# Performance work log

Hardware: AMD Instinct MI355X
Metric: run time of the kernel (lower is better)

Reference implementation:

```python
import jax, jax.numpy as jnp
import numpy as np

WIN = (7, 7)
NUM_HEADS = 12
DIM = 384
HEAD_DIM = DIM // NUM_HEADS
SCALE = HEAD_DIM ** (-0.5)


def _relative_position_index(wh, ww):
    coords = np.stack(np.meshgrid(np.arange(wh), np.arange(ww), indexing='ij'))  # (2, wh, ww)
    cf = coords.reshape(2, -1)                                                    # (2, N)
    rel = cf[:, :, None] - cf[:, None, :]                                         # (2, N, N)
    rel = rel.transpose(1, 2, 0).astype(np.int64)
    rel[:, :, 0] += wh - 1
    rel[:, :, 1] += ww - 1
    rel[:, :, 0] *= 2 * ww - 1
    return rel.sum(-1).astype(np.int32)                                           # (N, N)


def setup_inputs() -> dict:
    key = jax.random.key(0)
    ks = jax.random.split(key, 5)
    B_, N, C = 4096, WIN[0] * WIN[1], DIM
    nW = 1024
    x = jax.random.normal(ks[0], (B_, N, C), dtype=jnp.float32)
    mask = jnp.zeros((nW, N, N), dtype=jnp.float32)  # 0/-inf additive mask; zeros here
    qkv_w = jax.random.normal(ks[1], (C, 3 * C), dtype=jnp.float32) * 0.02
    qkv_b = jnp.zeros((3 * C,), dtype=jnp.float32)
    proj_w = jax.random.normal(ks[2], (C, C), dtype=jnp.float32) * 0.02
    proj_b = jnp.zeros((C,), dtype=jnp.float32)
    table_size = (2 * WIN[0] - 1) * (2 * WIN[1] - 1)
    rpb_table = jax.random.normal(ks[3], (table_size, NUM_HEADS), dtype=jnp.float32) * 0.02
    rel_index = jnp.asarray(_relative_position_index(*WIN))
    return {"x": x, "mask": mask, "qkv_w": qkv_w, "qkv_b": qkv_b,
            "proj_w": proj_w, "proj_b": proj_b, "rpb_table": rpb_table,
            "rel_index": rel_index}


def reference(x, mask, qkv_w, qkv_b, proj_w, proj_b, rpb_table, rel_index):
    B_, N, C = x.shape
    H, Dh = NUM_HEADS, HEAD_DIM
    qkv = x @ qkv_w + qkv_b                                   # (B_, N, 3C)
    qkv = qkv.reshape(B_, N, 3, H, Dh).transpose(2, 0, 3, 1, 4)
    q, k, v = qkv[0], qkv[1], qkv[2]                          # each (B_, H, N, Dh)
    attn = jnp.einsum('bhnd,bhmd->bhnm', q * SCALE, k)        # (B_, H, N, N)
    # gathered relative position bias -> (H, N, N)
    bias = rpb_table[rel_index.reshape(-1)].reshape(N, N, H).transpose(2, 0, 1)
    attn = attn + bias[None]
    nW = mask.shape[0]
    attn = attn.reshape(B_ // nW, nW, H, N, N) + mask[None, :, None]
    attn = attn.reshape(B_, H, N, N)
    attn = jax.nn.softmax(attn, axis=-1)
    out = jnp.einsum('bhnm,bhmd->bhnd', attn, v)              # (B_, H, N, Dh)
    out = out.transpose(0, 2, 1, 3).reshape(B_, N, C)
    return out @ proj_w + proj_b
```

## Files before the change

kernel.cpp:

```cpp
#include <hip/hip_runtime.h>


#define NWIN 4096
#define NW_MASK 1024
#define NH 12
#define DIM 384
#define HD 32
#define NT 49
#define SCALEF 0.17677669529663687f

typedef __attribute__((ext_vector_type(4))) float f32x4;
typedef __attribute__((ext_vector_type(8))) __bf16 bf16x8;
typedef __attribute__((ext_vector_type(4))) unsigned int u32x4;

#define MFMA16(A, B, C) __builtin_amdgcn_mfma_f32_16x16x32_bf16( \
    __builtin_bit_cast(bf16x8, A), __builtin_bit_cast(bf16x8, B), (C), 0, 0, 0)

__device__ __forceinline__ void split2(float x0, float x1, unsigned& h, unsigned& l) {
    unsigned b0 = __float_as_uint(x0), b1 = __float_as_uint(x1);
    unsigned m0 = b0 & 0xffff0000u, m1 = b1 & 0xffff0000u;
    h = m1 | (m0 >> 16);
    float r0 = x0 - __uint_as_float(m0);
    float r1 = x1 - __uint_as_float(m1);
    l = (__float_as_uint(r1) & 0xffff0000u) | (__float_as_uint(r0) >> 16);
}

__device__ __forceinline__ void cvt8(const float4& a, const float4& c,
                                     u32x4& hi, u32x4& lo) {
    unsigned h0, l0, h1, l1, h2, l2, h3, l3;
    split2(a.x, a.y, h0, l0);
    split2(a.z, a.w, h1, l1);
    split2(c.x, c.y, h2, l2);
    split2(c.z, c.w, h3, l3);
    hi = u32x4{h0, h1, h2, h3};
    lo = u32x4{l0, l1, l2, l3};
}

__global__ __launch_bounds__(256)
void conv_w(const float* __restrict__ qkv_w, const float* __restrict__ proj_w,
            u32x4* __restrict__ wf)
{
    int tg = blockIdx.x * 256 + threadIdx.x;
    int fid = tg >> 6, lane = tg & 63;
    int kt = fid / 96, ntc = fid - kt * 96;
    const float* src; int ncols, n; u32x4* dst;
    if (ntc < 72) {
        src = qkv_w; ncols = 3 * DIM; n = ntc * 16 + (lane & 15);
        dst = wf + (size_t)((kt * 72 + ntc) * 128);
    } else {
        int nt2 = ntc - 72;
        src = proj_w; ncols = DIM; n = nt2 * 16 + (lane & 15);
        dst = wf + (size_t)(12 * 72 * 128) + (size_t)((kt * 24 + nt2) * 128);
    }
    int k0 = kt * 32 + ((lane >> 4) << 3);
    float e[8];
    #pragma unroll
    for (int j = 0; j < 8; ++j) e[j] = src[(size_t)(k0 + j) * ncols + n];
    float4 a = make_float4(e[0], e[1], e[2], e[3]);
    float4 c = make_float4(e[4], e[5], e[6], e[7]);
    u32x4 hi, lo; cvt8(a, c, hi, lo);
    dst[lane] = hi; dst[64 + lane] = lo;
}

__global__ __launch_bounds__(256, 3)
void attn_mfma(const float* __restrict__ x,
               const float* __restrict__ mask,
               const float* __restrict__ qkv_b,
               const float* __restrict__ rpb,
               const int* __restrict__ rel,
               const u32x4* __restrict__ wf,
               float* __restrict__ y)
{
    __shared__ __align__(16) float qs[2][NT * 36];
    __shared__ __align__(16) float ks[2][NT * 36];
    __shared__ __align__(16) float vT[2][HD * 52];
    __shared__ __align__(16) float lg[NT * 52];

    const int b = blockIdx.x;
    const int t = threadIdx.x;
    const int lane = t & 63;
    const int wid = t >> 6;
    const int h_l = wid >> 1;
    const int mhalf = wid & 1;
    const int lrow = lane & 15;
    const int lk8 = (lane >> 4) << 3;
    const int lr4 = (lane >> 4) << 2;
    const float* xb = x + (size_t)b * (NT * DIM);
    const float* mrow = mask + (size_t)(b & (NW_MASK - 1)) * (NT * NT);
    const u32x4* wfl = wf + lane;

    for (int pass = 0; pass < 6; ++pass) {
        const int h = pass * 2 + h_l;
        int gnt[6];
        #pragma unroll
        for (int ln = 0; ln < 6; ++ln)
            gnt[ln] = (ln >> 1) * 24 + 2 * h + (ln & 1);

        f32x4 acc[2][6];
        #pragma unroll
        for (int mt = 0; mt < 2; ++mt)
            #pragma unroll
            for (int ln = 0; ln < 6; ++ln)
                acc[mt][ln] = f32x4{0.f, 0.f, 0.f, 0.f};

        for (int kt = 0; kt < 12; ++kt) {
            u32x4 ah[2], al[2];
            #pragma unroll
            for (int mt = 0; mt < 2; ++mt) {
                int row = mhalf * 32 + mt * 16 + lrow;
                float4 a = make_float4(0.f, 0.f, 0.f, 0.f);
                float4 c = make_float4(0.f, 0.f, 0.f, 0.f);
                if (row < NT) {
                    const float4* px = (const float4*)(xb + row * DIM + kt * 32 + lk8);
                    a = px[0]; c = px[1];
                }
                cvt8(a, c, ah[mt], al[mt]);
            }
            #pragma unroll
            for (int ln = 0; ln < 6; ++ln) {
                const u32x4* bp = wfl + (kt * 72 + gnt[ln]) * 128;
                u32x4 bh = bp[0], bl = bp[64];
                #pragma unroll
                for (int mt = 0; mt < 2; ++mt) {
                    acc[mt][ln] = MFMA16(al[mt], bh, acc[mt][ln]);
                    acc[mt][ln] = MFMA16(ah[mt], bl, acc[mt][ln]);
                    acc[mt][ln] = MFMA16(ah[mt], bh, acc[mt][ln]);
                }
            }
        }

        #pragma unroll
        for (int ln = 0; ln < 6; ++ln) {
            int cc = ln * 16 + lrow;
            int p = cc >> 5, d = cc & 31;
            float bias = qkv_b[p * DIM + h * HD + d];
            #pragma unroll
            for (int mt = 0; mt < 2; ++mt) {
                #pragma unroll
                for (int r = 0; r < 4; ++r) {
                    int row = mhalf * 32 + mt * 16 + lr4 + r;
                    if (row < NT) {
                        float v = acc[mt][ln][r] + bias;
                        if (p == 0)      qs[h_l][row * 36 + d] = v * SCALEF;
                        else if (p == 1) ks[h_l][row * 36 + d] = v;
                        else             vT[h_l][d * 52 + row] = v;
                    }
                }
            }
        }
        __syncthreads();

        for (int hh = 0; hh < 2; ++hh) {
            const int hg = pass * 2 + hh;
            for (int idx = t; idx < NT * NT; idx += 256) {
                int n = idx / NT, m = idx - n * NT;
                const float4* q4 = (const float4*)&qs[hh][n * 36];
                const float4* k4 = (const float4*)&ks[hh][m * 36];
                float s = 0.f;
                #pragma unroll
                for (int u = 0; u < 8; ++u) {
                    float4 qa = q4[u], ka = k4[u];
                    s += qa.x * ka.x + qa.y * ka.y + qa.z * ka.z + qa.w * ka.w;
                }
                s += rpb[rel[idx] * NH + hg] + mrow[idx];
                lg[n * 52 + m] = s;
            }
            __syncthreads();
            if (t < NT) {
                float mx = -1e30f;
                for (int m = 0; m < NT; ++m) mx = fmaxf(mx, lg[t * 52 + m]);
                float sum = 0.f;
                for (int m = 0; m < NT; ++m) {
                    float e = __expf(lg[t * 52 + m] - mx);
                    lg[t * 52 + m] = e; sum += e;
                }
                float inv = 1.f / sum;
                for (int m = 0; m < NT; ++m) lg[t * 52 + m] *= inv;
            }
            __syncthreads();
            for (int idx = t; idx < NT * HD; idx += 256) {
                int n = idx >> 5, dd = idx & 31;
                const float4* p4 = (const float4*)&lg[n * 52];
                const float4* v4 = (const float4*)&vT[hh][dd * 52];
                float s = 0.f;
                #pragma unroll
                for (int u = 0; u < 12; ++u) {
                    float4 pa = p4[u], va = v4[u];
                    s += pa.x * va.x + pa.y * va.y + pa.z * va.z + pa.w * va.w;
                }
                s += lg[n * 52 + 48] * vT[hh][dd * 52 + 48];
                y[((size_t)b * NT + n) * DIM + hg * HD + dd] = s;
            }
            __syncthreads();
        }
    }
}

__global__ __launch_bounds__(256)
void proj_mfma(const u32x4* __restrict__ pwf,
               const float* __restrict__ proj_b,
               float* __restrict__ y)
{
    const int t = threadIdx.x;
    const int lane = t & 63;
    const int wid = t >> 6;
    const int mhalf = wid >> 1, nhalf = wid & 1;
    const int lrow = lane & 15;
    const int lk8 = (lane >> 4) << 3;
    const int lr4 = (lane >> 4) << 2;
    float* yb = y + (size_t)blockIdx.x * (64 * DIM);
    const u32x4* pwl = pwf + lane;

    f32x4 acc[2][12];
    #pragma unroll
    for (int mt = 0; mt < 2; ++mt)
        #pragma unroll
        for (int ln = 0; ln < 12; ++ln)
            acc[mt][ln] = f32x4{0.f, 0.f, 0.f, 0.f};

    for (int kt = 0; kt < 12; ++kt) {
        u32x4 ah[2], al[2];
        #pragma unroll
        for (int mt = 0; mt < 2; ++mt) {
            int row = mhalf * 32 + mt * 16 + lrow;
            const float4* px = (const float4*)(yb + row * DIM + kt * 32 + lk8);
            float4 a = px[0], c = px[1];
            cvt8(a, c, ah[mt], al[mt]);
        }
        #pragma unroll
        for (int ln = 0; ln < 12; ++ln) {
            const u32x4* bp = pwl + (kt * 24 + nhalf * 12 + ln) * 128;
            u32x4 bh = bp[0], bl = bp[64];
            #pragma unroll
            for (int mt = 0; mt < 2; ++mt) {
                acc[mt][ln] = MFMA16(al[mt], bh, acc[mt][ln]);
                acc[mt][ln] = MFMA16(ah[mt], bl, acc[mt][ln]);
                acc[mt][ln] = MFMA16(ah[mt], bh, acc[mt][ln]);
            }
        }
    }
    __syncthreads();
    #pragma unroll
    for (int ln = 0; ln < 12; ++ln) {
        int col = (nhalf * 12 + ln) * 16 + lrow;
        float bias = proj_b[col];
        #pragma unroll
        for (int mt = 0; mt < 2; ++mt)
            #pragma unroll
            for (int r = 0; r < 4; ++r) {
                int row = mhalf * 32 + mt * 16 + lr4 + r;
                yb[row * DIM + col] = acc[mt][ln][r] + bias;
            }
    }
}

#define HD_P 33
#define CHUNK 128
#define THREADS_A 384

__global__ __launch_bounds__(THREADS_A)
void win_attn_kernel(const float* __restrict__ x,
                     const float* __restrict__ mask,
                     const float* __restrict__ qkv_w,
                     const float* __restrict__ qkv_b,
                     const float* __restrict__ rpb,
                     const int*   __restrict__ rel,
                     float* __restrict__ y)
{
    __shared__ float xs[NT * CHUNK];
    __shared__ float qs[NT * HD_P];
    __shared__ float ks_[NT * HD_P];
    __shared__ float vs[NT * HD_P];
    __shared__ float lg[NT * NT];

    const int b = blockIdx.x;
    const int t = threadIdx.x;
    const float* xb = x + (size_t)b * (NT * DIM);
    const float* mrow = mask + (size_t)(b & (NW_MASK - 1)) * (NT * NT);

    const int tx = t % 96;
    const int ty = t / 96;
    const int p  = tx / 32;
    const int d  = tx % 32;

    for (int h = 0; h < NH; ++h) {
        float acc[13];
        #pragma unroll
        for (int i = 0; i < 13; ++i) acc[i] = 0.f;
        const int wcol = p * DIM + h * HD + d;

        for (int c = 0; c < 3; ++c) {
            __syncthreads();
            for (int i = t; i < NT * (CHUNK / 4); i += THREADS_A) {
                int r = i >> 5;
                int j = i & 31;
                ((float4*)xs)[i] = ((const float4*)xb)[r * 96 + c * 32 + j];
            }
            __syncthreads();
            const float4* xs4 = (const float4*)xs;
            const float* wb = qkv_w + (size_t)(c * CHUNK) * (3 * DIM) + wcol;
            for (int kk4 = 0; kk4 < CHUNK / 4; ++kk4) {
                float w0 = wb[(size_t)(kk4 * 4 + 0) * (3 * DIM)];
                float w1 = wb[(size_t)(kk4 * 4 + 1) * (3 * DIM)];
                float w2 = wb[(size_t)(kk4 * 4 + 2) * (3 * DIM)];
                float w3 = wb[(size_t)(kk4 * 4 + 3) * (3 * DIM)];
                #pragma unroll
                for (int i = 0; i < 13; ++i) {
                    int r = ty + 4 * i;
                    if (r < NT) {
                        float4 xv = xs4[r * 32 + kk4];
                        acc[i] += xv.x * w0;
                        acc[i] += xv.y * w1;
                        acc[i] += xv.z * w2;
                        acc[i] += xv.w * w3;
                    }
                }
            }
        }
        float bv = qkv_b[wcol];
        float* dst = (p == 0) ? qs : (p == 1) ? ks_ : vs;
        #pragma unroll
        for (int i = 0; i < 13; ++i) {
            int r = ty + 4 * i;
            if (r < NT) dst[r * HD_P + d] = acc[i] + bv;
        }
        __syncthreads();

        for (int idx = t; idx < NT * NT; idx += THREADS_A) {
            int n = idx / NT, m = idx % NT;
            float s = 0.f;
            #pragma unroll
            for (int kk = 0; kk < HD; ++kk)
                s += qs[n * HD_P + kk] * ks_[m * HD_P + kk];
            s = s * SCALEF + rpb[rel[idx] * NH + h] + mrow[idx];
            lg[idx] = s;
        }
        __syncthreads();

        if (t < NT) {
            float mx = -1e30f;
            for (int m = 0; m < NT; ++m) mx = fmaxf(mx, lg[t * NT + m]);
            float sum = 0.f;
            for (int m = 0; m < NT; ++m) {
                float e = __expf(lg[t * NT + m] - mx);
                lg[t * NT + m] = e;
                sum += e;
            }
            float inv = 1.f / sum;
            for (int m = 0; m < NT; ++m) lg[t * NT + m] *= inv;
        }
        __syncthreads();

        for (int idx = t; idx < NT * HD; idx += THREADS_A) {
            int n = idx >> 5, dd = idx & 31;
            float s = 0.f;
            #pragma unroll
            for (int m = 0; m < NT; ++m)
                s += lg[n * NT + m] * vs[m * HD_P + dd];
            y[(size_t)b * (NT * DIM) + n * DIM + h * HD + dd] = s;
        }
    }
}

#define RPB 16
__global__ __launch_bounds__(384)
void proj_kernel(const float* __restrict__ proj_w,
                 const float* __restrict__ proj_b,
                 float* __restrict__ y)
{
    __shared__ float ys[RPB * DIM];
    const int t = threadIdx.x;
    float* base = y + (size_t)blockIdx.x * (RPB * DIM);
    for (int i = t; i < RPB * DIM / 4; i += 384)
        ((float4*)ys)[i] = ((const float4*)base)[i];
    __syncthreads();

    float acc[RPB];
    #pragma unroll
    for (int i = 0; i < RPB; ++i) acc[i] = 0.f;
    const float* wp = proj_w + t;
    const float4* ys4 = (const float4*)ys;
    for (int kk4 = 0; kk4 < DIM / 4; ++kk4) {
        float w0 = wp[(kk4 * 4 + 0) * DIM];
        float w1 = wp[(kk4 * 4 + 1) * DIM];
        float w2 = wp[(kk4 * 4 + 2) * DIM];
        float w3 = wp[(kk4 * 4 + 3) * DIM];
        #pragma unroll
        for (int i = 0; i < RPB; ++i) {
            float4 xv = ys4[i * 96 + kk4];
            acc[i] += xv.x * w0 + xv.y * w1 + xv.z * w2 + xv.w * w3;
        }
    }
    float bv = proj_b[t];
    #pragma unroll
    for (int i = 0; i < RPB; ++i)
        base[i * DIM + t] = acc[i] + bv;
}

extern "C" void kernel_launch(void* const* d_in, const int* in_sizes, int n_in,
                              void* d_out, int out_size, void* d_ws, size_t ws_size,
                              hipStream_t stream) {
    const float* x      = (const float*)d_in[0];
    const float* mask   = (const float*)d_in[1];
    const float* qkv_w  = (const float*)d_in[2];
    const float* qkv_b  = (const float*)d_in[3];
    const float* proj_w = (const float*)d_in[4];
    const float* proj_b = (const float*)d_in[5];
    const float* rpb    = (const float*)d_in[6];
    const int*   rel    = (const int*)d_in[7];
    float* out = (float*)d_out;

    const size_t WS_NEED = (size_t)(12 * 96 * 128) * 16;
    if (d_ws != nullptr && ws_size >= WS_NEED) {
        u32x4* wf = (u32x4*)d_ws;
        conv_w<<<288, 256, 0, stream>>>(qkv_w, proj_w, wf);
        attn_mfma<<<NWIN, 256, 0, stream>>>(x, mask, qkv_b, rpb, rel, wf, out);
        proj_mfma<<<(NWIN * NT) / 64, 256, 0, stream>>>(wf + (size_t)(12 * 72 * 128), proj_b, out);
    } else {
        win_attn_kernel<<<NWIN, THREADS_A, 0, stream>>>(x, mask, qkv_w, qkv_b, rpb, rel, out);
        proj_kernel<<<(NWIN * NT) / RPB, 384, 0, stream>>>(proj_w, proj_b, out);
    }
}
```

Before: 2.209 ms.

## Register-resident fused attention per head pair with fp16 QK dot products

Replaces the three shared-memory-synchronized phases (logits, single-thread-per-row softmax, PV) with one phase in which 8-thread groups own 4 query rows each. Both heads of a pass are processed at once, using fp16 Q/K with fdot2, shuffle-based softmax reductions and shuffle-broadcast PV accumulation. The relative position bias is pregathered into a per-head table inside the weight conversion kernel, which removes the indirect gather. This cuts barriers and serial softmax work, at the cost of fp16 precision on QK, more registers and some idle threads, since only 208 of 256 are active.

```diff
diff --git a/kernel.cpp b/kernel.cpp
--- a/kernel.cpp
+++ b/kernel.cpp
@@ -12,9 +12,26 @@
 typedef __attribute__((ext_vector_type(4))) float f32x4;
 typedef __attribute__((ext_vector_type(8))) __bf16 bf16x8;
 typedef __attribute__((ext_vector_type(4))) unsigned int u32x4;
+typedef __attribute__((ext_vector_type(2))) _Float16 h2;
 
 #define MFMA16(A, B, C) __builtin_amdgcn_mfma_f32_16x16x32_bf16( \
     __builtin_bit_cast(bf16x8, A), __builtin_bit_cast(bf16x8, B), (C), 0, 0, 0)
+
+#if defined(__has_builtin)
+#if __has_builtin(__builtin_amdgcn_fdot2)
+#define HAS_FDOT2 1
+#endif
+#endif
+
+__device__ __forceinline__ float fdot2u(unsigned a, unsigned b, float c) {
+#ifdef HAS_FDOT2
+    return __builtin_amdgcn_fdot2(__builtin_bit_cast(h2, a),
+                                  __builtin_bit_cast(h2, b), c, false);
+#else
+    h2 av = __builtin_bit_cast(h2, a), bv = __builtin_bit_cast(h2, b);
+    return c + (float)av.x * (float)bv.x + (float)av.y * (float)bv.y;
+#endif
+}
 
 __device__ __forceinline__ void split2(float x0, float x1, unsigned& h, unsigned& l) {
     unsigned b0 = __float_as_uint(x0), b1 = __float_as_uint(x1);
@@ -27,54 +44,62 @@
 
 __device__ __forceinline__ void cvt8(const float4& a, const float4& c,
                                      u32x4& hi, u32x4& lo) {
-    unsigned h0, l0, h1, l1, h2, l2, h3, l3;
+    unsigned h0, l0, h1, l1, h2_, l2, h3, l3;
     split2(a.x, a.y, h0, l0);
     split2(a.z, a.w, h1, l1);
-    split2(c.x, c.y, h2, l2);
+    split2(c.x, c.y, h2_, l2);
     split2(c.z, c.w, h3, l3);
-    hi = u32x4{h0, h1, h2, h3};
+    hi = u32x4{h0, h1, h2_, h3};
     lo = u32x4{l0, l1, l2, l3};
 }
 
 __global__ __launch_bounds__(256)
 void conv_w(const float* __restrict__ qkv_w, const float* __restrict__ proj_w,
-            u32x4* __restrict__ wf)
+            const float* __restrict__ rpb, const int* __restrict__ rel,
+            u32x4* __restrict__ wf, float* __restrict__ biasT)
 {
-    int tg = blockIdx.x * 256 + threadIdx.x;
-    int fid = tg >> 6, lane = tg & 63;
-    int kt = fid / 96, ntc = fid - kt * 96;
-    const float* src; int ncols, n; u32x4* dst;
-    if (ntc < 72) {
-        src = qkv_w; ncols = 3 * DIM; n = ntc * 16 + (lane & 15);
-        dst = wf + (size_t)((kt * 72 + ntc) * 128);
+    if (blockIdx.x < 288) {
+        int tg = blockIdx.x * 256 + threadIdx.x;
+        int fid = tg >> 6, lane = tg & 63;
+        int kt = fid / 96, ntc = fid - kt * 96;
+        const float* src; int ncols, n; u32x4* dst;
+        if (ntc < 72) {
+            src = qkv_w; ncols = 3 * DIM; n = ntc * 16 + (lane & 15);
+            dst = wf + (size_t)((kt * 72 + ntc) * 128);
+        } else {
+            int nt2 = ntc - 72;
+            src = proj_w; ncols = DIM; n = nt2 * 16 + (lane & 15);
+            dst = wf + (size_t)(12 * 72 * 128) + (size_t)((kt * 24 + nt2) * 128);
+        }
+        int k0 = kt * 32 + ((lane >> 4) << 3);
+        float e[8];
+        #pragma unroll
+        for (int j = 0; j < 8; ++j) e[j] = src[(size_t)(k0 + j) * ncols + n];
+        float4 a = make_float4(e[0], e[1], e[2], e[3]);
+        float4 c = make_float4(e[4], e[5], e[6], e[7]);
+        u32x4 hi, lo; cvt8(a, c, hi, lo);
+        dst[lane] = hi; dst[64 + lane] = lo;
     } else {
-        int nt2 = ntc - 72;
-        src = proj_w; ncols = DIM; n = nt2 * 16 + (lane & 15);
-        dst = wf + (size_t)(12 * 72 * 128) + (size_t)((kt * 24 + nt2) * 128);
-    }
-    int k0 = kt * 32 + ((lane >> 4) << 3);
-    float e[8];
-    #pragma unroll
-    for (int j = 0; j < 8; ++j) e[j] = src[(size_t)(k0 + j) * ncols + n];
-    float4 a = make_float4(e[0], e[1], e[2], e[3]);
-    float4 c = make_float4(e[4], e[5], e[6], e[7]);
-    u32x4 hi, lo; cvt8(a, c, hi, lo);
-    dst[lane] = hi; dst[64 + lane] = lo;
+        int tid = (blockIdx.x - 288) * 256 + threadIdx.x;
+        if (tid < NH * NT * NT) {
+            int h = tid / (NT * NT);
+            int idx = tid - h * (NT * NT);
+            biasT[tid] = rpb[rel[idx] * NH + h];
+        }
+    }
 }
 
 __global__ __launch_bounds__(256, 3)
 void attn_mfma(const float* __restrict__ x,
                const float* __restrict__ mask,
                const float* __restrict__ qkv_b,
-               const float* __restrict__ rpb,
-               const int* __restrict__ rel,
+               const float* __restrict__ biasT,
                const u32x4* __restrict__ wf,
                float* __restrict__ y)
 {
-    __shared__ __align__(16) float qs[2][NT * 36];
-    __shared__ __align__(16) float ks[2][NT * 36];
-    __shared__ __align__(16) float vT[2][HD * 52];
-    __shared__ __align__(16) float lg[NT * 52];
+    __shared__ __align__(16) _Float16 qs16[2][NT * 56];
+    __shared__ __align__(16) _Float16 ks16[2][NT * 56];
+    __shared__ __align__(16) float    vs[2][NT * 36];
 
     const int b = blockIdx.x;
     const int t = threadIdx.x;
@@ -89,6 +114,14 @@
     const float* mrow = mask + (size_t)(b & (NW_MASK - 1)) * (NT * NT);
     const u32x4* wfl = wf + lane;
 
+    const int g  = t >> 3;
+    const int j8 = t & 7;
+    const int hh = (g < 13) ? 0 : 1;
+    const int rq = g - hh * 13;
+    const int n0 = rq * 4;
+    const int nrows = (rq == 12) ? 1 : 4;
+    const bool act = g < 26;
+
     for (int pass = 0; pass < 6; ++pass) {
         const int h = pass * 2 + h_l;
         int gnt[6];
@@ -129,6 +162,8 @@
             }
         }
 
+        __syncthreads();
+
         #pragma unroll
         for (int ln = 0; ln < 6; ++ln) {
             int cc = ln * 16 + lrow;
@@ -141,62 +176,122 @@
                     int row = mhalf * 32 + mt * 16 + lr4 + r;
                     if (row < NT) {
                         float v = acc[mt][ln][r] + bias;
-                        if (p == 0)      qs[h_l][row * 36 + d] = v * SCALEF;
-                        else if (p == 1) ks[h_l][row * 36 + d] = v;
-                        else             vT[h_l][d * 52 + row] = v;
+                        if (p == 0)      qs16[h_l][row * 56 + d] = (_Float16)(v * SCALEF);
+                        else if (p == 1) ks16[h_l][row * 56 + d] = (_Float16)v;
+                        else             vs[h_l][row * 36 + d] = v;
                     }
                 }
             }
         }
         __syncthreads();
 
-        for (int hh = 0; hh < 2; ++hh) {
+        if (act) {
             const int hg = pass * 2 + hh;
-            for (int idx = t; idx < NT * NT; idx += 256) {
-                int n = idx / NT, m = idx - n * NT;
-                const float4* q4 = (const float4*)&qs[hh][n * 36];
-                const float4* k4 = (const float4*)&ks[hh][m * 36];
-                float s = 0.f;
+            const float* bT = biasT + hg * (NT * NT);
+
+            unsigned qreg[4][16];
+            #pragma unroll
+            for (int r = 0; r < 4; ++r) {
+                if (r < nrows) {
+                    const u32x4* qp = (const u32x4*)&qs16[hh][(n0 + r) * 56];
+                    #pragma unroll
+                    for (int w = 0; w < 4; ++w) {
+                        u32x4 qv = qp[w];
+                        qreg[r][w * 4 + 0] = qv[0];
+                        qreg[r][w * 4 + 1] = qv[1];
+                        qreg[r][w * 4 + 2] = qv[2];
+                        qreg[r][w * 4 + 3] = qv[3];
+                    }
+                }
+            }
+
+            float P[4][7];
+            #pragma unroll
+            for (int i = 0; i < 7; ++i) {
+                int m = j8 + 8 * i;
+                bool vm = m < NT;
+                u32x4 kw0{}, kw1{}, kw2{}, kw3{};
+                if (vm) {
+                    const u32x4* kp = (const u32x4*)&ks16[hh][m * 56];
+                    kw0 = kp[0]; kw1 = kp[1]; kw2 = kp[2]; kw3 = kp[3];
+                }
                 #pragma unroll
-                for (int u = 0; u < 8; ++u) {
-                    float4 qa = q4[u], ka = k4[u];
-                    s += qa.x * ka.x + qa.y * ka.y + qa.z * ka.z + qa.w * ka.w;
-                }
-                s += rpb[rel[idx] * NH + hg] + mrow[idx];
-                lg[n * 52 + m] = s;
-            }
-            __syncthreads();
-            if (t < NT) {
-                float mx = -1e30f;
-                for (int m = 0; m < NT; ++m) mx = fmaxf(mx, lg[t * 52 + m]);
-                float sum = 0.f;
-                for (int m = 0; m < NT; ++m) {
-                    float e = __expf(lg[t * 52 + m] - mx);
-                    lg[t * 52 + m] = e; sum += e;
-                }
-                float inv = 1.f / sum;
-                for (int m = 0; m < NT; ++m) lg[t * 52 + m] *= inv;
-            }
-            __syncthreads();
-            for (int idx = t; idx < NT * HD; idx += 256) {
-                int n = idx >> 5, dd = idx & 31;
-                const float4* p4 = (const float4*)&lg[n * 52];
-                const float4* v4 = (const float4*)&vT[hh][dd * 52];
-                float s = 0.f;
+                for (int r = 0; r < 4; ++r) {
+                    if (r < nrows) {
+                        float lv = -1e30f;
+                        if (vm) {
+                            float dsum = 0.f;
+                            #pragma unroll
+                            for (int c = 0; c < 4; ++c) dsum = fdot2u(qreg[r][c], kw0[c], dsum);
+                            #pragma unroll
+                            for (int c = 0; c < 4; ++c) dsum = fdot2u(qreg[r][4 + c], kw1[c], dsum);
+                            #pragma unroll
+                            for (int c = 0; c < 4; ++c) dsum = fdot2u(qreg[r][8 + c], kw2[c], dsum);
+                            #pragma unroll
+                            for (int c = 0; c < 4; ++c) dsum = fdot2u(qreg[r][12 + c], kw3[c], dsum);
+                            int idx = (n0 + r) * NT + m;
+                            lv = dsum + bT[idx] + mrow[idx];
+                        }
+                        P[r][i] = lv;
+                    }
+                }
+            }
+
+            #pragma unroll
+            for (int r = 0; r < 4; ++r) {
+                if (r < nrows) {
+                    float mx = P[r][0];
+                    #pragma unroll
+                    for (int i = 1; i < 7; ++i) mx = fmaxf(mx, P[r][i]);
+                    mx = fmaxf(mx, __shfl_xor(mx, 1, 8));
+                    mx = fmaxf(mx, __shfl_xor(mx, 2, 8));
+                    mx = fmaxf(mx, __shfl_xor(mx, 4, 8));
+                    float sm = 0.f;
+                    #pragma unroll
+                    for (int i = 0; i < 7; ++i) {
+                        float e = __expf(P[r][i] - mx);
+                        P[r][i] = e; sm += e;
+                    }
+                    sm += __shfl_xor(sm, 1, 8);
+                    sm += __shfl_xor(sm, 2, 8);
+                    sm += __shfl_xor(sm, 4, 8);
+                    float inv = 1.f / sm;
+                    #pragma unroll
+                    for (int i = 0; i < 7; ++i) P[r][i] *= inv;
+                }
+            }
+
+            f32x4 oacc[4];
+            #pragma unroll
+            for (int r = 0; r < 4; ++r) oacc[r] = f32x4{0.f, 0.f, 0.f, 0.f};
+            #pragma unroll
+            for (int i8 = 0; i8 < 7; ++i8) {
                 #pragma unroll
-                for (int u = 0; u < 12; ++u) {
-                    float4 pa = p4[u], va = v4[u];
-                    s += pa.x * va.x + pa.y * va.y + pa.z * va.z + pa.w * va.w;
-                }
-                s += lg[n * 52 + 48] * vT[hh][dd * 52 + 48];
-                y[((size_t)b * NT + n) * DIM + hg * HD + dd] = s;
-            }
-            __syncthreads();
-        }
-    }
-}
-
-__global__ __launch_bounds__(256)
+                for (int jj = 0; jj < 8; ++jj) {
+                    const int mm = i8 * 8 + jj;
+                    if (mm < NT) {
+                        f32x4 v4 = *(const f32x4*)&vs[hh][mm * 36 + j8 * 4];
+                        #pragma unroll
+                        for (int r = 0; r < 4; ++r) {
+                            if (r < nrows) {
+                                float p = __shfl(P[r][i8], jj, 8);
+                                oacc[r] += v4 * p;
+                            }
+                        }
+                    }
+                }
+            }
+            #pragma unroll
+            for (int r = 0; r < 4; ++r) {
+                if (r < nrows) {
+                    *(f32x4*)&y[((size_t)b * NT + (n0 + r)) * DIM + hg * HD + j8 * 4] = oacc[r];
+                }
+            }
+        }
+    }
+}
+
+__global__ __launch_bounds__(256, 3)
 void proj_mfma(const u32x4* __restrict__ pwf,
                const float* __restrict__ proj_b,
                float* __restrict__ y)
@@ -270,7 +365,7 @@
     __shared__ float xs[NT * CHUNK];
     __shared__ float qs[NT * HD_P];
     __shared__ float ks_[NT * HD_P];
-    __shared__ float vs[NT * HD_P];
+    __shared__ float vsf[NT * HD_P];
     __shared__ float lg[NT * NT];
 
     const int b = blockIdx.x;
@@ -318,7 +413,7 @@
             }
         }
         float bv = qkv_b[wcol];
-        float* dst = (p == 0) ? qs : (p == 1) ? ks_ : vs;
+        float* dst = (p == 0) ? qs : (p == 1) ? ks_ : vsf;
         #pragma unroll
         for (int i = 0; i < 13; ++i) {
             int r = ty + 4 * i;
@@ -356,7 +451,7 @@
             float s = 0.f;
             #pragma unroll
             for (int m = 0; m < NT; ++m)
-                s += lg[n * NT + m] * vs[m * HD_P + dd];
+                s += lg[n * NT + m] * vsf[m * HD_P + dd];
             y[(size_t)b * (NT * DIM) + n * DIM + h * HD + dd] = s;
         }
     }
@@ -410,11 +505,13 @@
     const int*   rel    = (const int*)d_in[7];
     float* out = (float*)d_out;
 
-    const size_t WS_NEED = (size_t)(12 * 96 * 128) * 16;
+    const size_t WS_FRAG = (size_t)(12 * 96 * 128) * 16;
+    const size_t WS_NEED = WS_FRAG + (size_t)NH * NT * NT * 4;
     if (d_ws != nullptr && ws_size >= WS_NEED) {
         u32x4* wf = (u32x4*)d_ws;
-        conv_w<<<288, 256, 0, stream>>>(qkv_w, proj_w, wf);
-        attn_mfma<<<NWIN, 256, 0, stream>>>(x, mask, qkv_b, rpb, rel, wf, out);
+        float* biasT = (float*)((char*)d_ws + WS_FRAG);
+        conv_w<<<401, 256, 0, stream>>>(qkv_w, proj_w, rpb, rel, wf, biasT);
+        attn_mfma<<<NWIN, 256, 0, stream>>>(x, mask, qkv_b, biasT, wf, out);
         proj_mfma<<<(NWIN * NT) / 64, 256, 0, stream>>>(wf + (size_t)(12 * 72 * 128), proj_b, out);
     } else {
         win_attn_kernel<<<NWIN, THREADS_A, 0, stream>>>(x, mask, qkv_w, qkv_b, rpb, rel, out);
```

Result: slower. 7.079 ms (+220.5%).
